# Performance work log

Hardware: AMD Instinct MI355X
Metric: run time of the kernel (lower is better)

Reference implementation:

```python
import jax, jax.numpy as jnp
import numpy as np


def setup_inputs() -> dict:
    key = jax.random.key(0)
    ks = jax.random.split(key, 4)
    B, H, W, C = 4, 64, 64, 64
    d = C // 8
    s = 0.05
    return {
        "x": jax.random.normal(ks[0], (B, H, W, C), dtype=jnp.float32),
        "Wq": jax.random.normal(ks[1], (C, d), dtype=jnp.float32) * s,
        "bq": jnp.zeros((d,), dtype=jnp.float32),
        "Wk": jax.random.normal(ks[2], (C, d), dtype=jnp.float32) * s,
        "bk": jnp.zeros((d,), dtype=jnp.float32),
        "Wv": jax.random.normal(ks[3], (C, C), dtype=jnp.float32) * s,
        "bv": jnp.zeros((C,), dtype=jnp.float32),
        "gamma": jnp.zeros((1,), dtype=jnp.float32),
    }


def reference(x, Wq, bq, Wk, bk, Wv, bv, gamma):
    B, H, W, C = x.shape
    N = H * W
    xt = x.reshape(B, N, C)  # tokens = flattened spatial positions
    # 1x1 convs == per-token matmuls
    q = xt @ Wq + bq          # [B, N, C//8]
    k = xt @ Wk + bk          # [B, N, C//8]
    v = xt @ Wv + bv          # [B, N, C]
    # unscaled QK^T softmax (SAGAN uses no 1/sqrt(d) scaling)
    attn = jax.nn.softmax(jnp.einsum('bnd,bmd->bnm', q, k), axis=-1)  # [B, N, N]
    out = jnp.einsum('bnm,bmc->bnc', attn, v).reshape(B, H, W, C)
    return gamma * out + x
```

## Files before the change

kernel.cpp:

```cpp
#include <hip/hip_runtime.h>
#include <hip/hip_bf16.h>


typedef __attribute__((ext_vector_type(4))) float f32x4;
typedef __attribute__((ext_vector_type(8))) short short8;

#define LOG2E 1.44269504088896340736f

#if __has_builtin(__builtin_amdgcn_exp2f)
#define EXP2(x) __builtin_amdgcn_exp2f(x)
#else
#define EXP2(x) __builtin_exp2f(x)
#endif

__device__ __forceinline__ float bf2f(unsigned short u) {
    union { unsigned int i; float f; } cv;
    cv.i = ((unsigned int)u) << 16;
    return cv.f;
}

__device__ __forceinline__ unsigned int pkbf_rnd(float lo, float hi) {
    union { float f; unsigned int u; } a, b;
    a.f = lo; b.f = hi;
    const unsigned int ar = a.u + 0x8000u;
    const unsigned int br = b.u + 0x8000u;
    return __builtin_amdgcn_perm(br, ar, 0x07060302u);
}

__device__ __forceinline__ unsigned char f2fp8(float v) {
    return (unsigned char)(__builtin_amdgcn_cvt_pk_fp8_f32(v, v, 0, false) & 0xFF);
}

__global__ __launch_bounds__(256) void sagan_proj_kernel(
    const float* __restrict__ x,
    const float* __restrict__ Wq, const float* __restrict__ bq,
    const float* __restrict__ Wk, const float* __restrict__ bk,
    const float* __restrict__ Wv, const float* __restrict__ bv,
    unsigned char* __restrict__ Q8, unsigned char* __restrict__ K8,
    unsigned char* __restrict__ V8, unsigned char* __restrict__ zp)
{
    const int tid  = threadIdx.x;
    const int lane = tid & 63;
    const int w    = tid >> 6;
    const int g    = lane >> 4;
    const int ql   = lane & 15;
    const int blk  = blockIdx.x;
    const int tglob0 = blk << 5;
    const int b    = tglob0 >> 12;
    const int nb   = tglob0 & 4095;
    const int chunk = nb >> 5;

    if (blk == 0 && tid < 16) zp[tid] = 0;

    short8 xa[2][2];
    #pragma unroll
    for (int t = 0; t < 2; ++t) {
        const float* xr = x + (size_t)(tglob0 + t * 16 + ql) * 64 + g * 8;
        #pragma unroll
        for (int s = 0; s < 2; ++s) {
            const f32x4 lo = *(const f32x4*)(xr + s * 32);
            const f32x4 hi = *(const f32x4*)(xr + s * 32 + 4);
            union { unsigned int u[4]; short8 v; } pk;
            pk.u[0] = pkbf_rnd(lo[0], lo[1]);
            pk.u[1] = pkbf_rnd(lo[2], lo[3]);
            pk.u[2] = pkbf_rnd(hi[0], hi[1]);
            pk.u[3] = pkbf_rnd(hi[2], hi[3]);
            xa[t][s] = pk.v;
        }
    }

    const f32x4 zc = {0.f, 0.f, 0.f, 0.f};

    {
        const int cp = w * 16 + ql;
        short8 bf[2];
        #pragma unroll
        for (int s = 0; s < 2; ++s) {
            const float* wp = Wv + (size_t)(s * 32 + g * 8) * 64 + cp;
            union { unsigned int u[4]; short8 v; } pk;
            #pragma unroll
            for (int jj = 0; jj < 4; ++jj)
                pk.u[jj] = pkbf_rnd(wp[(jj * 2) * 64], wp[(jj * 2 + 1) * 64]);
            bf[s] = pk.v;
        }
        const float bvc = bv[cp];
        #pragma unroll
        for (int t = 0; t < 2; ++t) {
            f32x4 acc = __builtin_amdgcn_mfma_f32_16x16x32_bf16(xa[t][0], bf[0], zc, 0, 0, 0);
            acc = __builtin_amdgcn_mfma_f32_16x16x32_bf16(xa[t][1], bf[1], acc, 0, 0, 0);
            int pk8 = __builtin_amdgcn_cvt_pk_fp8_f32(acc[0] + bvc, acc[1] + bvc, 0, false);
            pk8     = __builtin_amdgcn_cvt_pk_fp8_f32(acc[2] + bvc, acc[3] + bvc, pk8, true);
            unsigned char* dst = V8 + ((size_t)((b * 128 + chunk) * 64 + cp)) * 32
                                    + t * 16 + g * 4;
            *(unsigned int*)dst = (unsigned int)pk8;
        }
    }

    if (w < 2) {
        short8 bqk[2];
        const bool isQ = (ql < 8);
        const int dcol = isQ ? ql : (ql - 8);
        #pragma unroll
        for (int s = 0; s < 2; ++s) {
            const float* wp = (isQ ? Wq : Wk) + (size_t)(s * 32 + g * 8) * 8 + dcol;
            const float sc = isQ ? LOG2E : 1.0f;
            union { unsigned int u[4]; short8 v; } pk;
            #pragma unroll
            for (int jj = 0; jj < 4; ++jj)
                pk.u[jj] = pkbf_rnd(wp[(jj * 2) * 8] * sc, wp[(jj * 2 + 1) * 8] * sc);
            bqk[s] = pk.v;
        }
        const float bias = isQ ? (bq[dcol] * LOG2E) : bk[dcol];
        f32x4 acc = __builtin_amdgcn_mfma_f32_16x16x32_bf16(xa[w][0], bqk[0], zc, 0, 0, 0);
        acc = __builtin_amdgcn_mfma_f32_16x16x32_bf16(xa[w][1], bqk[1], acc, 0, 0, 0);
        unsigned char* base = (isQ ? Q8 : K8)
                            + (size_t)(tglob0 + w * 16 + g * 4) * 8 + dcol;
        #pragma unroll
        for (int r = 0; r < 4; ++r)
            base[r * 8] = f2fp8(acc[r] + bias);
    }
}


#define SOFTMAX_PA(KA0, KA1, QF, LL, PA) do {                                 \
    const f32x4 zc = {0.f, 0.f, 0.f, 0.f};                                    \
    f32x4 s0 = __builtin_amdgcn_mfma_f32_16x16x32_fp8_fp8(KA0, QF, zc, 0,0,0);\
    f32x4 s1 = __builtin_amdgcn_mfma_f32_16x16x32_fp8_fp8(KA1, QF, zc, 0,0,0);\
    float p[8];                                                               \
    _Pragma("unroll")                                                         \
    for (int r = 0; r < 4; ++r) {                                             \
        p[r]     = EXP2(s0[r]);                                               \
        p[4 + r] = EXP2(s1[r]);                                               \
    }                                                                         \
    LL += ((p[0] + p[1]) + (p[2] + p[3])) + ((p[4] + p[5]) + (p[6] + p[7]));  \
    union { int i[2]; long l; } pk;                                           \
    pk.i[0] = __builtin_amdgcn_cvt_pk_fp8_f32(p[0], p[1], 0, false);          \
    pk.i[0] = __builtin_amdgcn_cvt_pk_fp8_f32(p[2], p[3], pk.i[0], true);     \
    pk.i[1] = __builtin_amdgcn_cvt_pk_fp8_f32(p[4], p[5], 0, false);          \
    pk.i[1] = __builtin_amdgcn_cvt_pk_fp8_f32(p[6], p[7], pk.i[1], true);     \
    PA = pk.l;                                                                \
} while (0)

__global__ __launch_bounds__(256, 4) void sagan_flash_kernel(
    const unsigned char* __restrict__ Q8, const unsigned char* __restrict__ K8,
    const unsigned char* __restrict__ V8, const unsigned char* __restrict__ zp,
    const float* __restrict__ x, const float* __restrict__ gamma_p,
    float* __restrict__ out)
{
    __shared__ unsigned short sacc[4][32][72];
    __shared__ float sl[4][32];

    const int tid  = threadIdx.x;
    const int lane = tid & 63;
    const int w    = tid >> 6;
    const int g    = lane >> 4;
    const int ql   = lane & 15;
    const int blk  = blockIdx.x;
    const int b    = blk >> 7;
    const int qbase = (blk & 127) << 5;

    const unsigned char* Kbase = K8 + (size_t)b * (4096 * 8);
    const unsigned char* Qbase = Q8 + (size_t)b * (4096 * 8);

    long qf0, qf1;
    {
        const unsigned char* qp = Qbase + (size_t)(qbase + ql) * 8;
        qf0 = (g == 0) ? *(const long*)(qp)       : 0L;
        qf1 = (g == 0) ? *(const long*)(qp + 128) : 0L;
    }

    const int kt0 = w << 10;

    const unsigned char* kp0;
    int kstep;
    if (g == 0) {
        const int kperm = ((ql >> 2) << 3) | (ql & 3);
        kp0 = Kbase + (size_t)(kt0 + kperm) * 8;
        kstep = 256;
    } else {
        kp0 = zp; kstep = 0;
    }

    const unsigned char* vp = V8 + (size_t)(b * 128 + w * 32) * 2048
                                 + ql * 32 + g * 8;

    f32x4 acc00 = {0.f,0.f,0.f,0.f}, acc01 = acc00, acc02 = acc00, acc03 = acc00;
    f32x4 acc10 = acc00, acc11 = acc00, acc12 = acc00, acc13 = acc00;
    float l0 = 0.f, l1 = 0.f;

    #pragma unroll 1
    for (int it = 0; it < 32; ++it) {
        const long ka0 = *(const long*)kp0;
        const long ka1 = *(const long*)(kp0 + 32);
        kp0 += kstep;
        const long vf0 = *(const long*)(vp);
        const long vf1 = *(const long*)(vp + 512);
        const long vf2 = *(const long*)(vp + 1024);
        const long vf3 = *(const long*)(vp + 1536);
        vp += 2048;

        __builtin_amdgcn_s_setprio(1);
        long pa0, pa1;
        SOFTMAX_PA(ka0, ka1, qf0, l0, pa0);
        SOFTMAX_PA(ka0, ka1, qf1, l1, pa1);
        acc00 = __builtin_amdgcn_mfma_f32_16x16x32_fp8_fp8(pa0, vf0, acc00, 0, 0, 0);
        acc10 = __builtin_amdgcn_mfma_f32_16x16x32_fp8_fp8(pa1, vf0, acc10, 0, 0, 0);
        acc01 = __builtin_amdgcn_mfma_f32_16x16x32_fp8_fp8(pa0, vf1, acc01, 0, 0, 0);
        acc11 = __builtin_amdgcn_mfma_f32_16x16x32_fp8_fp8(pa1, vf1, acc11, 0, 0, 0);
        acc02 = __builtin_amdgcn_mfma_f32_16x16x32_fp8_fp8(pa0, vf2, acc02, 0, 0, 0);
        acc12 = __builtin_amdgcn_mfma_f32_16x16x32_fp8_fp8(pa1, vf2, acc12, 0, 0, 0);
        acc03 = __builtin_amdgcn_mfma_f32_16x16x32_fp8_fp8(pa0, vf3, acc03, 0, 0, 0);
        acc13 = __builtin_amdgcn_mfma_f32_16x16x32_fp8_fp8(pa1, vf3, acc13, 0, 0, 0);
        __builtin_amdgcn_s_setprio(0);
    }

    l0 += __shfl_xor(l0, 16); l0 += __shfl_xor(l0, 32);
    l1 += __shfl_xor(l1, 16); l1 += __shfl_xor(l1, 32);

    #pragma unroll
    for (int r = 0; r < 4; ++r) {
        const int row = (g << 2) | r;
        unsigned short* d0 = &sacc[w][row][0];
        d0[ql]      = (unsigned short)(pkbf_rnd(acc00[r], acc00[r]) & 0xFFFF);
        d0[16 + ql] = (unsigned short)(pkbf_rnd(acc01[r], acc01[r]) & 0xFFFF);
        d0[32 + ql] = (unsigned short)(pkbf_rnd(acc02[r], acc02[r]) & 0xFFFF);
        d0[48 + ql] = (unsigned short)(pkbf_rnd(acc03[r], acc03[r]) & 0xFFFF);
        unsigned short* d1 = &sacc[w][16 + row][0];
        d1[ql]      = (unsigned short)(pkbf_rnd(acc10[r], acc10[r]) & 0xFFFF);
        d1[16 + ql] = (unsigned short)(pkbf_rnd(acc11[r], acc11[r]) & 0xFFFF);
        d1[32 + ql] = (unsigned short)(pkbf_rnd(acc12[r], acc12[r]) & 0xFFFF);
        d1[48 + ql] = (unsigned short)(pkbf_rnd(acc13[r], acc13[r]) & 0xFFFF);
    }
    if (g == 0) {
        sl[w][ql] = l0; sl[w][16 + ql] = l1;
    }
    __syncthreads();

    {
        const int row = tid >> 3;
        const int cg  = (tid & 7) * 8;
        float L = 0.f;
        float O[8] = {0.f, 0.f, 0.f, 0.f, 0.f, 0.f, 0.f, 0.f};
        #pragma unroll
        for (int ww = 0; ww < 4; ++ww) {
            L += sl[ww][row];
            const uint4 v = *(const uint4*)&sacc[ww][row][cg];
            O[0] += bf2f((unsigned short)(v.x & 0xFFFF));
            O[1] += bf2f((unsigned short)(v.x >> 16));
            O[2] += bf2f((unsigned short)(v.y & 0xFFFF));
            O[3] += bf2f((unsigned short)(v.y >> 16));
            O[4] += bf2f((unsigned short)(v.z & 0xFFFF));
            O[5] += bf2f((unsigned short)(v.z >> 16));
            O[6] += bf2f((unsigned short)(v.w & 0xFFFF));
            O[7] += bf2f((unsigned short)(v.w >> 16));
        }
        const float Li = 1.0f / L;
        const float gm = gamma_p[0];
        const size_t off = ((size_t)(b * 4096 + qbase + row)) * 64 + cg;
        const f32x4 xv0 = *(const f32x4*)(x + off);
        const f32x4 xv1 = *(const f32x4*)(x + off + 4);
        f32x4 o0, o1;
        o0[0] = gm * (O[0] * Li) + xv0[0];
        o0[1] = gm * (O[1] * Li) + xv0[1];
        o0[2] = gm * (O[2] * Li) + xv0[2];
        o0[3] = gm * (O[3] * Li) + xv0[3];
        o1[0] = gm * (O[4] * Li) + xv1[0];
        o1[1] = gm * (O[5] * Li) + xv1[1];
        o1[2] = gm * (O[6] * Li) + xv1[2];
        o1[3] = gm * (O[7] * Li) + xv1[3];
        *(f32x4*)(out + off)     = o0;
        *(f32x4*)(out + off + 4) = o1;
    }
}

extern "C" void kernel_launch(void* const* d_in, const int* in_sizes, int n_in,
                              void* d_out, int out_size, void* d_ws, size_t ws_size,
                              hipStream_t stream) {
    const float* x  = (const float*)d_in[0];
    const float* Wq = (const float*)d_in[1];
    const float* bq = (const float*)d_in[2];
    const float* Wk = (const float*)d_in[3];
    const float* bk = (const float*)d_in[4];
    const float* Wv = (const float*)d_in[5];
    const float* bv = (const float*)d_in[6];
    const float* gm = (const float*)d_in[7];
    float* out = (float*)d_out;

    unsigned char* Q8 = (unsigned char*)d_ws;
    unsigned char* K8 = Q8 + 131072;
    unsigned char* V8 = K8 + 131072;
    unsigned char* zp = V8 + 1048576;

    hipLaunchKernelGGL(sagan_proj_kernel, dim3(512), dim3(256), 0, stream,
                       x, Wq, bq, Wk, bk, Wv, bv, Q8, K8, V8, zp);
    hipLaunchKernelGGL(sagan_flash_kernel, dim3(512), dim3(256), 0, stream,
                       Q8, K8, V8, zp, x, gm, out);
}
```

Before: 33.42 us.

## Split flash attention key range across 16 waves per block instead of 4

Each block now runs 1024 threads (16 waves), and each wave processes a quarter as many key tiles (8 iterations instead of 32). The partial accumulators from all 16 waves are reduced through a larger shared-memory buffer, and 512 threads write the output. The aim is more parallelism and latency hiding within each query tile, since the grid of 512 blocks may leave CUs underfilled. The cost is a larger cross-wave reduction, more LDS use (about 74KB) and fewer resident blocks per CU.

```diff
diff --git a/kernel.cpp b/kernel.cpp
--- a/kernel.cpp
+++ b/kernel.cpp
@@ -141,14 +141,14 @@
     PA = pk.l;                                                                \
 } while (0)
 
-__global__ __launch_bounds__(256, 4) void sagan_flash_kernel(
+__global__ __launch_bounds__(1024, 4) void sagan_flash_kernel(
     const unsigned char* __restrict__ Q8, const unsigned char* __restrict__ K8,
     const unsigned char* __restrict__ V8, const unsigned char* __restrict__ zp,
     const float* __restrict__ x, const float* __restrict__ gamma_p,
     float* __restrict__ out)
 {
-    __shared__ unsigned short sacc[4][32][72];
-    __shared__ float sl[4][32];
+    __shared__ unsigned short sacc[16][32][72];
+    __shared__ float sl[16][32];
 
     const int tid  = threadIdx.x;
     const int lane = tid & 63;
@@ -169,7 +169,7 @@
         qf1 = (g == 0) ? *(const long*)(qp + 128) : 0L;
     }
 
-    const int kt0 = w << 10;
+    const int kt0 = w << 8;
 
     const unsigned char* kp0;
     int kstep;
@@ -181,7 +181,7 @@
         kp0 = zp; kstep = 0;
     }
 
-    const unsigned char* vp = V8 + (size_t)(b * 128 + w * 32) * 2048
+    const unsigned char* vp = V8 + (size_t)(b * 128 + w * 8) * 2048
                                  + ql * 32 + g * 8;
 
     f32x4 acc00 = {0.f,0.f,0.f,0.f}, acc01 = acc00, acc02 = acc00, acc03 = acc00;
@@ -189,7 +189,7 @@
     float l0 = 0.f, l1 = 0.f;
 
     #pragma unroll 1
-    for (int it = 0; it < 32; ++it) {
+    for (int it = 0; it < 8; ++it) {
         const long ka0 = *(const long*)kp0;
         const long ka1 = *(const long*)(kp0 + 32);
         kp0 += kstep;
@@ -236,40 +236,30 @@
     }
     __syncthreads();
 
-    {
-        const int row = tid >> 3;
-        const int cg  = (tid & 7) * 8;
+    if (tid < 512) {
+        const int row = tid >> 4;
+        const int c4  = tid & 15;
         float L = 0.f;
-        float O[8] = {0.f, 0.f, 0.f, 0.f, 0.f, 0.f, 0.f, 0.f};
-        #pragma unroll
-        for (int ww = 0; ww < 4; ++ww) {
+        float O[4] = {0.f, 0.f, 0.f, 0.f};
+        #pragma unroll
+        for (int ww = 0; ww < 16; ++ww) {
             L += sl[ww][row];
-            const uint4 v = *(const uint4*)&sacc[ww][row][cg];
+            const uint2 v = *(const uint2*)&sacc[ww][row][c4 * 4];
             O[0] += bf2f((unsigned short)(v.x & 0xFFFF));
             O[1] += bf2f((unsigned short)(v.x >> 16));
             O[2] += bf2f((unsigned short)(v.y & 0xFFFF));
             O[3] += bf2f((unsigned short)(v.y >> 16));
-            O[4] += bf2f((unsigned short)(v.z & 0xFFFF));
-            O[5] += bf2f((unsigned short)(v.z >> 16));
-            O[6] += bf2f((unsigned short)(v.w & 0xFFFF));
-            O[7] += bf2f((unsigned short)(v.w >> 16));
         }
         const float Li = 1.0f / L;
         const float gm = gamma_p[0];
-        const size_t off = ((size_t)(b * 4096 + qbase + row)) * 64 + cg;
-        const f32x4 xv0 = *(const f32x4*)(x + off);
-        const f32x4 xv1 = *(const f32x4*)(x + off + 4);
-        f32x4 o0, o1;
-        o0[0] = gm * (O[0] * Li) + xv0[0];
-        o0[1] = gm * (O[1] * Li) + xv0[1];
-        o0[2] = gm * (O[2] * Li) + xv0[2];
-        o0[3] = gm * (O[3] * Li) + xv0[3];
-        o1[0] = gm * (O[4] * Li) + xv1[0];
-        o1[1] = gm * (O[5] * Li) + xv1[1];
-        o1[2] = gm * (O[6] * Li) + xv1[2];
-        o1[3] = gm * (O[7] * Li) + xv1[3];
-        *(f32x4*)(out + off)     = o0;
-        *(f32x4*)(out + off + 4) = o1;
+        const size_t off = ((size_t)(b * 4096 + qbase + row)) * 64 + c4 * 4;
+        const f32x4 xv = *(const f32x4*)(x + off);
+        f32x4 o;
+        o[0] = gm * (O[0] * Li) + xv[0];
+        o[1] = gm * (O[1] * Li) + xv[1];
+        o[2] = gm * (O[2] * Li) + xv[2];
+        o[3] = gm * (O[3] * Li) + xv[3];
+        *(f32x4*)(out + off) = o;
     }
 }
 
@@ -293,6 +283,6 @@
 
     hipLaunchKernelGGL(sagan_proj_kernel, dim3(512), dim3(256), 0, stream,
                        x, Wq, bq, Wk, bk, Wv, bv, Q8, K8, V8, zp);
-    hipLaunchKernelGGL(sagan_flash_kernel, dim3(512), dim3(256), 0, stream,
+    hipLaunchKernelGGL(sagan_flash_kernel, dim3(512), dim3(1024), 0, stream,
                        Q8, K8, V8, zp, x, gm, out);
 }
```

After: 30.95 us. 1.08x faster.
